# Performance work log

Measured on AMD Instinct MI355X. Metric: run time of the kernel, lower is better.

The kernel has to match this reference:

```python
import jax, jax.numpy as jnp
import numpy as np

B, C, L, D, P, Q = 8, 32, 512, 128, 96, 3
LEVELS = 3
ORDERS = [1, 2, 3, 4]  # begin_order=1 + band index

# db4 decomposition low-pass filter (pywt convention)
_LO = np.array([-0.010597401784997278, 0.032883011666982945,
                0.030841381835986965, -0.18703481171888114,
                -0.02798376941698385, 0.6308807679295904,
                0.7148465705525415, 0.23037781330885523], dtype=np.float32)
FLEN = int(_LO.size)
_HI = (_LO[::-1] * ((-1.0) ** (np.arange(FLEN) + 1))).astype(np.float32)

DEC_LO_R = jnp.asarray(_LO[::-1].copy())  # correlation kernel = reversed dec_lo
DEC_HI_R = jnp.asarray(_HI[::-1].copy())
REC_LO_R = jnp.asarray(_LO.copy())        # rec_lo[::-1] == dec_lo (orthogonal wavelet)
REC_HI_R = jnp.asarray(_HI.copy())        # rec_hi[::-1] == dec_hi


def _corr(x, k, stride=1, pad=0):
    # batched 1D correlation; x: [N, Lx], k: [flen]
    return jax.lax.conv_general_dilated(
        x[:, None, :], k[None, None, :], (stride,), [(pad, pad)],
        dimension_numbers=('NCH', 'OIH', 'NCH'))[:, 0, :]


def dwt_step(x):
    # pywt.dwt, mode='symmetric': half-sample symmetric extension by flen-1,
    # correlate with reversed filter, sample odd positions. out len = (n+flen-1)//2
    p = FLEN - 1
    ext = jnp.concatenate([x[:, :p][:, ::-1], x, x[:, -p:][:, ::-1]], axis=1)
    e = ext[:, 1:]
    return _corr(e, DEC_LO_R, stride=2), _corr(e, DEC_HI_R, stride=2)


def idwt_step(a, d):
    # pywt.idwt: upsample-by-2, full convolution with rec filters, trim flen-2 per side
    n = a.shape[1]
    z = jnp.zeros((a.shape[0], 2 * n - 1), a.dtype)
    ua = z.at[:, ::2].set(a)
    ud = z.at[:, ::2].set(d)
    y = _corr(ua, REC_LO_R, pad=FLEN - 1) + _corr(ud, REC_HI_R, pad=FLEN - 1)
    t = FLEN - 2
    return y[:, t:y.shape[1] - t]


def dwt_bands(x):
    # x: [N, L] -> LEVELS+1 single-band reconstructions (wavedec + selective waverec)
    n = x.shape[1]
    a, dets = x, []
    for _ in range(LEVELS):
        a, d = dwt_step(a)
        dets.append(d)
    clist = [a] + dets[::-1]  # [cA_L, cD_L, ..., cD_1]
    bands = []
    for i in range(len(clist)):
        keep = [c if j == i else jnp.zeros_like(c) for j, c in enumerate(clist)]
        r = keep[0]
        for d in keep[1:]:
            if r.shape[1] == d.shape[1] + 1:  # pywt waverec length fixup
                r = r[:, :-1]
            r = idwt_step(r, d)
        bands.append(r[:, :n])
    return bands


def embed(x1, w):
    # TokenEmbedding: Conv1d(1, D, k=3, padding=1, circular, bias=False); x_mark=None
    xp = jnp.concatenate([x1[:, -1:], x1, x1[:, :1]], axis=1)[:, None, :]
    y = jax.lax.conv_general_dilated(xp, w, (1,), [(0, 0)],
                                     dimension_numbers=('NCH', 'OIH', 'NCH'))
    return y.transpose(0, 2, 1)  # [N, L, D]


def cheby(x, coeffs):
    # ChebyKANLinear: tanh squash, Chebyshev T_0..T_K-1 recurrence, contract with coeffs
    # x: [M, Din], coeffs: [Din, Dout, K]
    x = jnp.tanh(x)
    K = coeffs.shape[2]
    t_prev = jnp.ones_like(x)
    out = t_prev @ coeffs[:, :, 0]
    if K > 1:
        t = x
        out = out + t @ coeffs[:, :, 1]
        for k in range(2, K):
            t, t_prev = 2.0 * x * t - t_prev, t
            out = out + t @ coeffs[:, :, k]
    return out


def conv_same(x, w, b, dil):
    # x: [N, Ch, L]; Conv1d(C, C, 3, padding=dil, dilation=dil)
    y = jax.lax.conv_general_dilated(x, w, (1,), [(dil, dil)], rhs_dilation=(dil,),
                                     dimension_numbers=('NCH', 'OIH', 'NCH'))
    return y + b[None, :, None]


def tcn(x, w1, b1, w2, b2, dil):
    h = x.transpose(0, 2, 1)
    h = jax.nn.gelu(conv_same(h, w1, b1, dil), approximate=False)
    h = jax.nn.gelu(conv_same(h, w2, b2, dil), approximate=False)
    return h.transpose(0, 2, 1) + x  # residual (dropout is eval-mode identity)


def _forward(x_enc, emb_w, chebs, tcns, proj_w, proj_b, pred_w, pred_b):
    bsz = x_enc.shape[0]
    # use_norm=0 -> Normalize is identity; original detaches before CPU DWT
    x = jax.lax.stop_gradient(x_enc)
    xc = x.transpose(0, 2, 1).reshape(bsz * C, L)  # per-channel series
    bands = dwt_bands(xc)
    fused = jnp.zeros((bsz * C, L, D), x_enc.dtype)
    for i, band in enumerate(bands):
        emb = embed(band, emb_w)  # [B*C, L, D]
        x1 = cheby(emb.reshape(-1, D), chebs[i]).reshape(bsz * C, L, D)
        dil = max(1, 2 ** max(ORDERS[i] - 1, 0))
        fused = fused + x1 + tcn(emb, *tcns[i], dil)
    # predict_layer over time, projection over features
    h = jnp.einsum('nld,pl->npd', fused, pred_w) + pred_b[None, :, None]  # [B*C, P, D]
    out = jnp.einsum('npd,qd->npq', h, proj_w) + proj_b                  # [B*C, P, Q]
    return out.reshape(bsz, C, P, Q)[:, 0]  # channel 0, denorm is identity


def setup_inputs() -> dict:
    key = jax.random.key(0)
    ks = iter(jax.random.split(key, 64))
    inp = {'x_enc': jax.random.normal(next(ks), (B, L, C), jnp.float32)}
    inp['emb_w'] = jax.random.normal(next(ks), (D, 1, 3), jnp.float32) * (2.0 / 3.0) ** 0.5
    std = (2.0 / (D * 3)) ** 0.5
    for i, o in enumerate(ORDERS):
        K = o + 1
        inp[f'cheb{i}'] = jax.random.normal(next(ks), (D, D, K), jnp.float32) * (1.0 / (D * K))
        inp[f'tw1_{i}'] = jax.random.normal(next(ks), (D, D, 3), jnp.float32) * std
        inp[f'tb1_{i}'] = jnp.zeros((D,), jnp.float32)
        inp[f'tw2_{i}'] = jax.random.normal(next(ks), (D, D, 3), jnp.float32) * std
        inp[f'tb2_{i}'] = jnp.zeros((D,), jnp.float32)
    inp['proj_w'] = jax.random.normal(next(ks), (Q, D), jnp.float32) * D ** -0.5
    inp['proj_b'] = jnp.zeros((Q,), jnp.float32)
    inp['pred_w'] = jax.random.normal(next(ks), (P, L), jnp.float32) * L ** -0.5
    inp['pred_b'] = jnp.zeros((P,), jnp.float32)
    return inp


def reference(x_enc, emb_w, cheb0, tw1_0, tb1_0, tw2_0, tb2_0,
              cheb1, tw1_1, tb1_1, tw2_1, tb2_1,
              cheb2, tw1_2, tb1_2, tw2_2, tb2_2,
              cheb3, tw1_3, tb1_3, tw2_3, tb2_3,
              proj_w, proj_b, pred_w, pred_b):
    chebs = [cheb0, cheb1, cheb2, cheb3]
    tcns = [(tw1_0, tb1_0, tw2_0, tb2_0), (tw1_1, tb1_1, tw2_1, tb2_1),
            (tw1_2, tb1_2, tw2_2, tb2_2), (tw1_3, tb1_3, tw2_3, tb2_3)]
    return _forward(x_enc, emb_w, chebs, tcns, proj_w, proj_b, pred_w, pred_b)
```

## Files before the change

kernel.cpp:

```cpp
#include <hip/hip_runtime.h>
#include <math.h>

#define NB 8
#define LL 512
#define DD 128
#define PP 96
#define QQ 3

#define WS_BANDS 0
#define WS_CFR   16384
#define WS_WFR   (WS_CFR + 114688)
#define WS_PWT   (WS_WFR + 196608)

typedef __attribute__((ext_vector_type(8))) short short8v;
typedef __attribute__((ext_vector_type(4))) float f32x4;

#define MFMA16(a, b, c) __builtin_amdgcn_mfma_f32_16x16x32_bf16(a, b, c, 0, 0, 0)

__device__ __forceinline__ short f2bf(float f) {
  unsigned u = __builtin_bit_cast(unsigned, f);
  unsigned r = (u + 0x7fffu + ((u >> 16) & 1u)) >> 16;
  return (short)r;
}

__device__ __forceinline__ float fast_tanh(float x) {
  float ax = fabsf(x);
  float e = __expf(-2.0f * ax);
  float r = (1.0f - e) * __builtin_amdgcn_rcpf(1.0f + e);
  return x < 0.0f ? -r : r;
}

__device__ __forceinline__ float fast_gelu(float x) {
  float u = 0.7978845608028654f * x * (1.0f + 0.044715f * x * x);
  return x * __builtin_amdgcn_rcpf(1.0f + __expf(-2.0f * u));
}

constexpr float W_LO[8] = {
  -0.010597401784997278f, 0.032883011666982945f, 0.030841381835986965f,
  -0.18703481171888114f, -0.02798376941698385f, 0.6308807679295904f,
  0.7148465705525415f, 0.23037781330885523f
};

__device__ void dwt_level(const float* xin, int n, float* a, float* d,
                          int tid, int nthr) {
  int outn = (n + 5) / 2 + 1;
  for (int j = tid; j < outn; j += nthr) {
    float sa = 0.f, sd = 0.f;
#pragma unroll
    for (int k = 0; k < 8; ++k) {
      int i = 2 * j + k;
      int idx = (i < 6) ? (5 - i) : ((i < n + 6) ? (i - 6) : (2 * n + 5 - i));
      float v = xin[idx];
      sa += v * W_LO[7 - k];
      sd += v * ((k & 1) ? -W_LO[k] : W_LO[k]);
    }
    a[j] = sa;
    d[j] = sd;
  }
}

__device__ void idwt_level(const float* a, const float* d, float* out, int n,
                           int tid, int nthr) {
  int outn = 2 * n - 6;
  for (int t = tid; t < outn; t += nthr) {
    float s = 0.f;
#pragma unroll
    for (int k = 0; k < 8; ++k) {
      int j = t - 1 + k;
      if (j >= 0 && j <= 2 * n - 2 && ((j & 1) == 0)) {
        int m = j >> 1;
        if (a) s += a[m] * W_LO[k];
        if (d) s += d[m] * ((k & 1) ? W_LO[7 - k] : -W_LO[7 - k]);
      }
    }
    out[t] = s;
  }
}

struct PrepArgs {
  const float* x_enc;
  const float* cheb[4];
  const float* w1[4];
  const float* w2[4];
  const float* pred_b;
  const float* pred_w;
  const float* proj_w;
  const float* proj_b;
  float* bands;
  short* cfr;
  short* wfr;
  float* pwt;
  float* out;
};

__global__ __launch_bounds__(256) void prep_kernel(PrepArgs a) {
  __shared__ float sx[LL];
  __shared__ float a1[259], d1[259], a2[133], d2[133], a3[70], d3[70];
  __shared__ float rA[LL], rB[LL];
  int bid = blockIdx.x, t = threadIdx.x;
  if (bid < 32) {
    int n = bid & 7, band = bid >> 3;
    for (int l = t; l < LL; l += 256)
      sx[l] = a.x_enc[(size_t)n * LL * 32 + (size_t)l * 32];
    __syncthreads();
    dwt_level(sx, 512, a1, d1, t, 256); __syncthreads();
    dwt_level(a1, 259, a2, d2, t, 256); __syncthreads();
    dwt_level(a2, 133, a3, d3, t, 256); __syncthreads();
    idwt_level(band == 0 ? a3 : nullptr, band == 1 ? d3 : nullptr, rA, 70, t, 256);
    __syncthreads();
    idwt_level(rA, band == 2 ? d2 : nullptr, rB, 133, t, 256);
    __syncthreads();
    idwt_level(rB, band == 3 ? d1 : nullptr, rA, 259, t, 256);
    __syncthreads();
    float* dstb = a.bands + ((size_t)band * NB + n) * LL;
    for (int l = t; l < LL; l += 256) dstb[l] = rA[l];
  } else if (bid < 160) {
    const int CFRG = 28672, WFRG = 49152, PWTN = LL * PP;
    const int total = CFRG + WFRG + PWTN;
    for (int g = (bid - 32) * 256 + t; g < total; g += 128 * 256) {
      if (g < CFRG) {
        int gs = g >> 11, r = g & 2047;
        int ks = r >> 9, r2 = r & 511;
        int nt = r2 >> 6, lane = r2 & 63;
        int b = (gs >= 9) ? 3 : ((gs >= 5) ? 2 : ((gs >= 2) ? 1 : 0));
        int off = (b == 3) ? 9 : ((b == 2) ? 5 : ((b == 1) ? 2 : 0));
        int kcoef = gs - off;
        int K = b + 2;
        int din0 = ks * 32 + (lane >> 4) * 8;
        int dout = nt * 16 + (lane & 15);
        const float* src = a.cheb[b];
        short8v v;
#pragma unroll
        for (int el = 0; el < 8; ++el)
          v[el] = f2bf(src[((size_t)(din0 + el) * DD + dout) * K + kcoef]);
        ((short8v*)a.cfr)[g] = v;
      } else if (g < CFRG + WFRG) {
        int g2 = g - CFRG;
        int m = g2 >> 11, r = g2 & 2047;
        int ks = r >> 9, r2 = r & 511;
        int nt = r2 >> 6, lane = r2 & 63;
        int bw = m / 3, tap = m - bw * 3;
        int band = bw >> 1, which = bw & 1;
        const float* w = which ? a.w2[band] : a.w1[band];
        int din0 = ks * 32 + (lane >> 4) * 8;
        int dout = nt * 16 + (lane & 15);
        short8v v;
#pragma unroll
        for (int el = 0; el < 8; ++el)
          v[el] = f2bf(w[((size_t)dout * DD + din0 + el) * 3 + tap]);
        ((short8v*)a.wfr)[g2] = v;
      } else {
        int e = g - CFRG - WFRG;
        int l = e / PP, p = e - l * PP;
        a.pwt[e] = a.pred_w[(size_t)p * LL + l];
      }
    }
  } else {
    __shared__ float S[4];
    if (t < QQ) {
      const float4* pw = (const float4*)(a.proj_w + (size_t)t * DD);
      float s = 0.f;
#pragma unroll
      for (int i = 0; i < 32; ++i) {
        float4 v = pw[i];
        s += v.x + v.y + v.z + v.w;
      }
      S[t] = s;
    }
    __syncthreads();
    for (int i = t; i < NB * PP * QQ; i += 256) {
      int pq = i % (PP * QQ);
      int p = pq / QQ, q = pq - p * QQ;
      a.out[i] = a.pred_b[p] * S[q] + a.proj_b[q];
    }
  }
}

struct MainArgs {
  const float* emb_w;
  const float* bands;
  const short* cfr;
  const short* wfr;
  const float* proj_w;
  const float* pwt;
  const float* b1[4];
  const float* b2[4];
  float* out;
};

__device__ __forceinline__ void proj_epilogue(
    const MainArgs& ar, int n, int l0, float* tile, float* red, float* gq) {
  int t = threadIdx.x;
  __syncthreads();
  if (t < 192) {
    int pair = t % 96, half = t / 96;
    int p_loc = pair / 3, q = pair - (pair / 3) * 3;
    const float* pw = ar.proj_w + (size_t)q * DD + half * 64;
    const float* tr = tile + p_loc * 132 + half * 64;
    float sv = 0.f;
#pragma unroll 8
    for (int d = 0; d < 64; ++d) sv += tr[d] * pw[d];
    red[t] = sv;
  }
  __syncthreads();
  if (t < 96) gq[t] = red[t] + red[96 + t];
  __syncthreads();
  if (t < PP) {
    const float* pw = ar.pwt + (size_t)l0 * PP + t;
    float s0 = 0.f, s1 = 0.f, s2 = 0.f;
#pragma unroll 8
    for (int l = 0; l < 32; ++l) {
      float w = pw[l * PP];
      s0 += w * gq[l * 3 + 0];
      s1 += w * gq[l * 3 + 1];
      s2 += w * gq[l * 3 + 2];
    }
    float* op = ar.out + (size_t)n * (PP * QQ) + t * 3;
    atomicAdd(op + 0, s0);
    atomicAdd(op + 1, s1);
    atomicAdd(op + 2, s2);
  }
}

template <int NS>
__device__ __forceinline__ void cheby_core(
    const MainArgs& ar, int band, int n, int l0, short* sU, float* blx,
    float* red, float* gq) {
  int t = threadIdx.x;
  const float* brow = ar.bands + ((size_t)band * NB + n) * LL;
  const float* ew = ar.emb_w;
  if (t < 34) blx[t] = brow[(l0 - 1 + t + LL) & 511];
  __syncthreads();
  for (int idx = t; idx < 32 * DD; idx += 256) {
    int l = idx >> 7, dch = idx & 127;
    float e = ew[dch * 3] * blx[l] + ew[dch * 3 + 1] * blx[l + 1] +
              ew[dch * 3 + 2] * blx[l + 2];
    float x = fast_tanh(e);
    int o = l * 136 + dch;
    sU[o] = f2bf(x);
    if (NS >= 3) {
      float t2 = 2.f * x * x - 1.f;
      sU[4352 + o] = f2bf(t2);
      if (NS >= 4) {
        float t3 = 2.f * x * t2 - x;
        sU[8704 + o] = f2bf(t3);
        if (NS >= 5) sU[13056 + o] = f2bf(2.f * x * t3 - t2);
      }
    }
  }
  __syncthreads();

  int w = t >> 6, lane = t & 63;
  int r16 = lane & 15, kq = lane >> 4;
  const int sbase = (NS - 2) * (NS + 1) / 2;
  const short8v* cfrv = (const short8v*)ar.cfr;
  const short ONEB = (short)0x3F80;
  short8v ones = {ONEB, ONEB, ONEB, ONEB, ONEB, ONEB, ONEB, ONEB};
  f32x4 cacc[2][2];
#pragma unroll
  for (int i = 0; i < 2; ++i)
#pragma unroll
    for (int j = 0; j < 2; ++j) cacc[i][j] = (f32x4){0.f, 0.f, 0.f, 0.f};
#pragma unroll
  for (int s = 0; s < NS; ++s) {
    short8v bfr0[4], bfr1[4];
#pragma unroll
    for (int ks = 0; ks < 4; ++ks) {
      bfr0[ks] = cfrv[(((sbase + s) * 4 + ks) * 8 + w * 2 + 0) * 64 + lane];
      bfr1[ks] = cfrv[(((sbase + s) * 4 + ks) * 8 + w * 2 + 1) * 64 + lane];
    }
#pragma unroll
    for (int ks = 0; ks < 4; ++ks) {
      short8v a0, a1;
      if (s == 0) {
        a0 = ones;
        a1 = ones;
      } else {
        a0 = *(const short8v*)&sU[(s - 1) * 4352 + r16 * 136 + ks * 32 + kq * 8];
        a1 = *(const short8v*)&sU[(s - 1) * 4352 + (16 + r16) * 136 + ks * 32 + kq * 8];
      }
      cacc[0][0] = MFMA16(a0, bfr0[ks], cacc[0][0]);
      cacc[0][1] = MFMA16(a0, bfr1[ks], cacc[0][1]);
      cacc[1][0] = MFMA16(a1, bfr0[ks], cacc[1][0]);
      cacc[1][1] = MFMA16(a1, bfr1[ks], cacc[1][1]);
    }
  }
  __syncthreads();
  float* tile = (float*)sU;
  int row0 = kq * 4;
#pragma unroll
  for (int nt = 0; nt < 2; ++nt) {
    int dout = w * 32 + nt * 16 + r16;
#pragma unroll
    for (int m = 0; m < 2; ++m)
#pragma unroll
      for (int r = 0; r < 4; ++r)
        tile[(m * 16 + row0 + r) * 132 + dout] = cacc[m][nt][r];
  }
  proj_epilogue(ar, n, l0, tile, red, gq);
}

template <int DIL>
__device__ __forceinline__ void conv_core(
    const MainArgs& ar, int band, int n, int l0, short* sU, float* blx2,
    float* red, float* gq) {
  int t = threadIdx.x;
  const float* brow = ar.bands + ((size_t)band * NB + n) * LL;
  const float* ew = ar.emb_w;
  if (t < 66) blx2[t] = brow[(l0 - 2 * DIL - 1 + t + LL) & 511];
  __syncthreads();

  const int ETR = 32 + 4 * DIL;
  for (int idx = t; idx < ETR * DD; idx += 256) {
    int v = idx >> 7, dch = idx & 127;
    int l = l0 - 2 * DIL + v;
    float e = 0.f;
    if (l >= 0 && l < LL)
      e = ew[dch * 3] * blx2[v] + ew[dch * 3 + 1] * blx2[v + 1] +
          ew[dch * 3 + 2] * blx2[v + 2];
    sU[v * 136 + dch] = f2bf(e);
  }
  __syncthreads();

  int w = t >> 6, lane = t & 63;
  int r16 = lane & 15, kq = lane >> 4;
  const short8v* wfrv = (const short8v*)ar.wfr;

  const int m3a = (band * 2) * 3;
  f32x4 acc1[3][2];
#pragma unroll
  for (int i = 0; i < 3; ++i)
#pragma unroll
    for (int j = 0; j < 2; ++j) acc1[i][j] = (f32x4){0.f, 0.f, 0.f, 0.f};
#pragma unroll
  for (int tap = 0; tap < 3; ++tap) {
    short8v bfr0[4], bfr1[4];
#pragma unroll
    for (int ks = 0; ks < 4; ++ks) {
      bfr0[ks] = wfrv[(((m3a + tap) * 4 + ks) * 8 + w * 2 + 0) * 64 + lane];
      bfr1[ks] = wfrv[(((m3a + tap) * 4 + ks) * 8 + w * 2 + 1) * 64 + lane];
    }
#pragma unroll
    for (int ks = 0; ks < 4; ++ks) {
#pragma unroll
      for (int m = 0; m < 3; ++m) {
        short8v av = *(const short8v*)&sU[(m * 16 + r16 + tap * DIL) * 136 + ks * 32 + kq * 8];
        acc1[m][0] = MFMA16(av, bfr0[ks], acc1[m][0]);
        acc1[m][1] = MFMA16(av, bfr1[ks], acc1[m][1]);
      }
    }
  }
  {
    float bias0 = ar.b1[band][w * 32 + r16];
    float bias1 = ar.b1[band][w * 32 + 16 + r16];
#pragma unroll
    for (int m = 0; m < 3; ++m)
#pragma unroll
      for (int r = 0; r < 4; ++r) {
        int u = m * 16 + kq * 4 + r;
        int l = l0 - DIL + u;
        bool valid = (l >= 0) && (l < LL) && (u < 32 + 2 * DIL);
        short v0 = valid ? f2bf(fast_gelu(acc1[m][0][r] + bias0)) : (short)0;
        short v1 = valid ? f2bf(fast_gelu(acc1[m][1][r] + bias1)) : (short)0;
        sU[8704 + u * 136 + w * 32 + r16] = v0;
        sU[8704 + u * 136 + w * 32 + 16 + r16] = v1;
      }
  }
  __syncthreads();

  const int m3b = (band * 2 + 1) * 3;
  f32x4 acc2[2][2];
#pragma unroll
  for (int i = 0; i < 2; ++i)
#pragma unroll
    for (int j = 0; j < 2; ++j) acc2[i][j] = (f32x4){0.f, 0.f, 0.f, 0.f};
#pragma unroll
  for (int tap = 0; tap < 3; ++tap) {
    short8v bfr0[4], bfr1[4];
#pragma unroll
    for (int ks = 0; ks < 4; ++ks) {
      bfr0[ks] = wfrv[(((m3b + tap) * 4 + ks) * 8 + w * 2 + 0) * 64 + lane];
      bfr1[ks] = wfrv[(((m3b + tap) * 4 + ks) * 8 + w * 2 + 1) * 64 + lane];
    }
#pragma unroll
    for (int ks = 0; ks < 4; ++ks) {
#pragma unroll
      for (int m = 0; m < 2; ++m) {
        short8v av = *(const short8v*)&sU[8704 + (m * 16 + r16 + tap * DIL) * 136 + ks * 32 + kq * 8];
        acc2[m][0] = MFMA16(av, bfr0[ks], acc2[m][0]);
        acc2[m][1] = MFMA16(av, bfr1[ks], acc2[m][1]);
      }
    }
  }

  float* tile = (float*)sU;
#pragma unroll
  for (int nt = 0; nt < 2; ++nt) {
    int dout = w * 32 + nt * 16 + r16;
    float b2v = ar.b2[band][dout];
    float w0 = ew[dout * 3], w1 = ew[dout * 3 + 1], w2 = ew[dout * 3 + 2];
#pragma unroll
    for (int m = 0; m < 2; ++m)
#pragma unroll
      for (int r = 0; r < 4; ++r) {
        int p = m * 16 + kq * 4 + r;
        float eres = w0 * blx2[p + 2 * DIL] + w1 * blx2[p + 2 * DIL + 1] +
                     w2 * blx2[p + 2 * DIL + 2];
        tile[p * 132 + dout] = fast_gelu(acc2[m][nt][r] + b2v) + eres;
      }
  }
  proj_epilogue(ar, n, l0, tile, red, gq);
}

__global__ __launch_bounds__(256) void main_kernel(MainArgs ar) {
  __shared__ __align__(16) short sU[17408];
  __shared__ float blx[80];
  __shared__ float red[192];
  __shared__ float gq[96];
  int bid = blockIdx.x;
  int role = bid & 1, band = (bid >> 1) & 3, n = (bid >> 3) & 7;
  int l0 = (bid >> 6) << 5;
  if (role == 0) {
    switch (band) {
      case 0: cheby_core<2>(ar, band, n, l0, sU, blx, red, gq); break;
      case 1: cheby_core<3>(ar, band, n, l0, sU, blx, red, gq); break;
      case 2: cheby_core<4>(ar, band, n, l0, sU, blx, red, gq); break;
      default: cheby_core<5>(ar, band, n, l0, sU, blx, red, gq); break;
    }
  } else {
    switch (band) {
      case 0: conv_core<1>(ar, band, n, l0, sU, blx, red, gq); break;
      case 1: conv_core<2>(ar, band, n, l0, sU, blx, red, gq); break;
      case 2: conv_core<4>(ar, band, n, l0, sU, blx, red, gq); break;
      default: conv_core<8>(ar, band, n, l0, sU, blx, red, gq); break;
    }
  }
}

extern "C" void kernel_launch(void* const* d_in, const int* in_sizes, int n_in,
                              void* d_out, int out_size, void* d_ws, size_t ws_size,
                              hipStream_t stream) {
  const float* emb_w = (const float*)d_in[1];
  const float* proj_w = (const float*)d_in[22];
  const float* proj_b = (const float*)d_in[23];
  const float* pred_w = (const float*)d_in[24];
  const float* pred_b = (const float*)d_in[25];
  float* ws = (float*)d_ws;
  float* bands = ws + WS_BANDS;
  short* cfr = (short*)(ws + WS_CFR);
  short* wfr = (short*)(ws + WS_WFR);
  float* pwt = ws + WS_PWT;
  float* out = (float*)d_out;

  PrepArgs pa;
  pa.x_enc = (const float*)d_in[0];
  for (int i = 0; i < 4; ++i) {
    pa.cheb[i] = (const float*)d_in[2 + 5 * i];
    pa.w1[i] = (const float*)d_in[3 + 5 * i];
    pa.w2[i] = (const float*)d_in[5 + 5 * i];
  }
  pa.pred_b = pred_b; pa.pred_w = pred_w; pa.proj_w = proj_w; pa.proj_b = proj_b;
  pa.bands = bands; pa.cfr = cfr; pa.wfr = wfr; pa.pwt = pwt; pa.out = out;

  MainArgs ma;
  ma.emb_w = emb_w; ma.bands = bands; ma.cfr = cfr; ma.wfr = wfr;
  ma.proj_w = proj_w; ma.pwt = pwt;
  for (int i = 0; i < 4; ++i) {
    ma.b1[i] = (const float*)d_in[4 + 5 * i];
    ma.b2[i] = (const float*)d_in[6 + 5 * i];
  }
  ma.out = out;

  prep_kernel<<<161, 256, 0, stream>>>(pa);
  main_kernel<<<1024, 256, 0, stream>>>(ma);
}
```

Baseline: 33.10 us.

## Replace output atomics with per-tile partials and a final reduction kernel

Each main-kernel block now writes its partial projection sums to a dedicated workspace slot instead of doing float atomicAdd into the output. A new small final kernel sums the 128 partials per output element and adds the bias term. The bias initialisation moves out of the prep kernel into this final kernel. The aim is to remove atomic contention and make the result deterministic, at the cost of a third kernel launch and extra global traffic for the partials.

```diff
diff --git a/kernel.cpp b/kernel.cpp
--- a/kernel.cpp
+++ b/kernel.cpp
@@ -11,6 +11,7 @@
 #define WS_CFR   16384
 #define WS_WFR   (WS_CFR + 114688)
 #define WS_PWT   (WS_WFR + 196608)
+#define WS_PO    (WS_PWT + 49152)
 
 typedef __attribute__((ext_vector_type(8))) short short8v;
 typedef __attribute__((ext_vector_type(4))) float f32x4;
@@ -82,15 +83,11 @@
   const float* cheb[4];
   const float* w1[4];
   const float* w2[4];
-  const float* pred_b;
   const float* pred_w;
-  const float* proj_w;
-  const float* proj_b;
   float* bands;
   short* cfr;
   short* wfr;
   float* pwt;
-  float* out;
 };
 
 __global__ __launch_bounds__(256) void prep_kernel(PrepArgs a) {
@@ -114,7 +111,7 @@
     __syncthreads();
     float* dstb = a.bands + ((size_t)band * NB + n) * LL;
     for (int l = t; l < LL; l += 256) dstb[l] = rA[l];
-  } else if (bid < 160) {
+  } else {
     const int CFRG = 28672, WFRG = 49152, PWTN = LL * PP;
     const int total = CFRG + WFRG + PWTN;
     for (int g = (bid - 32) * 256 + t; g < total; g += 128 * 256) {
@@ -155,24 +152,6 @@
         a.pwt[e] = a.pred_w[(size_t)p * LL + l];
       }
     }
-  } else {
-    __shared__ float S[4];
-    if (t < QQ) {
-      const float4* pw = (const float4*)(a.proj_w + (size_t)t * DD);
-      float s = 0.f;
-#pragma unroll
-      for (int i = 0; i < 32; ++i) {
-        float4 v = pw[i];
-        s += v.x + v.y + v.z + v.w;
-      }
-      S[t] = s;
-    }
-    __syncthreads();
-    for (int i = t; i < NB * PP * QQ; i += 256) {
-      int pq = i % (PP * QQ);
-      int p = pq / QQ, q = pq - p * QQ;
-      a.out[i] = a.pred_b[p] * S[q] + a.proj_b[q];
-    }
   }
 }
 
@@ -185,11 +164,12 @@
   const float* pwt;
   const float* b1[4];
   const float* b2[4];
-  float* out;
+  float* po;
 };
 
 __device__ __forceinline__ void proj_epilogue(
-    const MainArgs& ar, int n, int l0, float* tile, float* red, float* gq) {
+    const MainArgs& ar, int sidx, int n, int l0, float* tile, float* red,
+    float* gq) {
   int t = threadIdx.x;
   __syncthreads();
   if (t < 192) {
@@ -215,17 +195,17 @@
       s1 += w * gq[l * 3 + 1];
       s2 += w * gq[l * 3 + 2];
     }
-    float* op = ar.out + (size_t)n * (PP * QQ) + t * 3;
-    atomicAdd(op + 0, s0);
-    atomicAdd(op + 1, s1);
-    atomicAdd(op + 2, s2);
+    float* op = ar.po + ((size_t)sidx * NB + n) * (PP * QQ) + t * 3;
+    op[0] = s0;
+    op[1] = s1;
+    op[2] = s2;
   }
 }
 
 template <int NS>
 __device__ __forceinline__ void cheby_core(
-    const MainArgs& ar, int band, int n, int l0, short* sU, float* blx,
-    float* red, float* gq) {
+    const MainArgs& ar, int band, int n, int l0, int sidx, short* sU,
+    float* blx, float* red, float* gq) {
   int t = threadIdx.x;
   const float* brow = ar.bands + ((size_t)band * NB + n) * LL;
   const float* ew = ar.emb_w;
@@ -297,13 +277,13 @@
       for (int r = 0; r < 4; ++r)
         tile[(m * 16 + row0 + r) * 132 + dout] = cacc[m][nt][r];
   }
-  proj_epilogue(ar, n, l0, tile, red, gq);
+  proj_epilogue(ar, sidx, n, l0, tile, red, gq);
 }
 
 template <int DIL>
 __device__ __forceinline__ void conv_core(
-    const MainArgs& ar, int band, int n, int l0, short* sU, float* blx2,
-    float* red, float* gq) {
+    const MainArgs& ar, int band, int n, int l0, int sidx, short* sU,
+    float* blx2, float* red, float* gq) {
   int t = threadIdx.x;
   const float* brow = ar.bands + ((size_t)band * NB + n) * LL;
   const float* ew = ar.emb_w;
@@ -409,7 +389,7 @@
         tile[p * 132 + dout] = fast_gelu(acc2[m][nt][r] + b2v) + eres;
       }
   }
-  proj_epilogue(ar, n, l0, tile, red, gq);
+  proj_epilogue(ar, sidx, n, l0, tile, red, gq);
 }
 
 __global__ __launch_bounds__(256) void main_kernel(MainArgs ar) {
@@ -419,21 +399,55 @@
   __shared__ float gq[96];
   int bid = blockIdx.x;
   int role = bid & 1, band = (bid >> 1) & 3, n = (bid >> 3) & 7;
-  int l0 = (bid >> 6) << 5;
+  int lt = bid >> 6;
+  int l0 = lt << 5;
+  int sidx = ((role << 2) | band) * 16 + lt;
   if (role == 0) {
     switch (band) {
-      case 0: cheby_core<2>(ar, band, n, l0, sU, blx, red, gq); break;
-      case 1: cheby_core<3>(ar, band, n, l0, sU, blx, red, gq); break;
-      case 2: cheby_core<4>(ar, band, n, l0, sU, blx, red, gq); break;
-      default: cheby_core<5>(ar, band, n, l0, sU, blx, red, gq); break;
+      case 0: cheby_core<2>(ar, band, n, l0, sidx, sU, blx, red, gq); break;
+      case 1: cheby_core<3>(ar, band, n, l0, sidx, sU, blx, red, gq); break;
+      case 2: cheby_core<4>(ar, band, n, l0, sidx, sU, blx, red, gq); break;
+      default: cheby_core<5>(ar, band, n, l0, sidx, sU, blx, red, gq); break;
     }
   } else {
     switch (band) {
-      case 0: conv_core<1>(ar, band, n, l0, sU, blx, red, gq); break;
-      case 1: conv_core<2>(ar, band, n, l0, sU, blx, red, gq); break;
-      case 2: conv_core<4>(ar, band, n, l0, sU, blx, red, gq); break;
-      default: conv_core<8>(ar, band, n, l0, sU, blx, red, gq); break;
-    }
+      case 0: conv_core<1>(ar, band, n, l0, sidx, sU, blx, red, gq); break;
+      case 1: conv_core<2>(ar, band, n, l0, sidx, sU, blx, red, gq); break;
+      case 2: conv_core<4>(ar, band, n, l0, sidx, sU, blx, red, gq); break;
+      default: conv_core<8>(ar, band, n, l0, sidx, sU, blx, red, gq); break;
+    }
+  }
+}
+
+__global__ __launch_bounds__(320) void final_kernel(
+    const float* __restrict__ po, const float* __restrict__ pred_b,
+    const float* __restrict__ proj_w, const float* __restrict__ proj_b,
+    float* __restrict__ out) {
+  __shared__ float S[4];
+  int n = blockIdx.x, t = threadIdx.x;
+  if (t < QQ) {
+    const float4* pw = (const float4*)(proj_w + (size_t)t * DD);
+    float s = 0.f;
+#pragma unroll
+    for (int i = 0; i < 32; ++i) {
+      float4 v = pw[i];
+      s += v.x + v.y + v.z + v.w;
+    }
+    S[t] = s;
+  }
+  __syncthreads();
+  if (t < PP * QQ) {
+    float s0 = 0.f, s1 = 0.f, s2 = 0.f, s3 = 0.f;
+#pragma unroll 4
+    for (int sl = 0; sl < 128; sl += 4) {
+      s0 += po[((size_t)(sl + 0) * NB + n) * (PP * QQ) + t];
+      s1 += po[((size_t)(sl + 1) * NB + n) * (PP * QQ) + t];
+      s2 += po[((size_t)(sl + 2) * NB + n) * (PP * QQ) + t];
+      s3 += po[((size_t)(sl + 3) * NB + n) * (PP * QQ) + t];
+    }
+    int p = t / QQ, q = t - p * QQ;
+    out[(size_t)n * (PP * QQ) + t] =
+        (s0 + s1) + (s2 + s3) + pred_b[p] * S[q] + proj_b[q];
   }
 }
 
@@ -450,6 +464,7 @@
   short* cfr = (short*)(ws + WS_CFR);
   short* wfr = (short*)(ws + WS_WFR);
   float* pwt = ws + WS_PWT;
+  float* po = ws + WS_PO;
   float* out = (float*)d_out;
 
   PrepArgs pa;
@@ -459,8 +474,8 @@
     pa.w1[i] = (const float*)d_in[3 + 5 * i];
     pa.w2[i] = (const float*)d_in[5 + 5 * i];
   }
-  pa.pred_b = pred_b; pa.pred_w = pred_w; pa.proj_w = proj_w; pa.proj_b = proj_b;
-  pa.bands = bands; pa.cfr = cfr; pa.wfr = wfr; pa.pwt = pwt; pa.out = out;
+  pa.pred_w = pred_w;
+  pa.bands = bands; pa.cfr = cfr; pa.wfr = wfr; pa.pwt = pwt;
 
   MainArgs ma;
   ma.emb_w = emb_w; ma.bands = bands; ma.cfr = cfr; ma.wfr = wfr;
@@ -469,8 +484,9 @@
     ma.b1[i] = (const float*)d_in[4 + 5 * i];
     ma.b2[i] = (const float*)d_in[6 + 5 * i];
   }
-  ma.out = out;
-
-  prep_kernel<<<161, 256, 0, stream>>>(pa);
+  ma.po = po;
+
+  prep_kernel<<<160, 256, 0, stream>>>(pa);
   main_kernel<<<1024, 256, 0, stream>>>(ma);
-}
+  final_kernel<<<NB, 320, 0, stream>>>(po, pred_b, proj_w, proj_b, out);
+}
```

Result: slower. 42.30 us (+27.8%).
